# Kernel optimization log

Hardware: AMD Instinct MI355X
Metric: run time of the kernel (lower is better)

The kernel has to match this reference:

```python
import jax, jax.numpy as jnp
import numpy as np

H = 16  # num_heads
THETA = 10000.0


def apply_rope(x, positions, theta=THETA):
    # x: [..., S, d_k]; positions: [S]
    d_k = x.shape[-1]
    inv_freq = theta ** (-jnp.arange(0, d_k, 2, dtype=jnp.float32) / d_k)  # [d_k/2]
    ang = positions.astype(jnp.float32)[:, None] * inv_freq[None, :]  # [S, d_k/2]
    cos, sin = jnp.cos(ang), jnp.sin(ang)
    x1 = x[..., 0::2]
    x2 = x[..., 1::2]
    out_even = x1 * cos - x2 * sin
    out_odd = x1 * sin + x2 * cos
    out = jnp.stack([out_even, out_odd], axis=-1)  # [..., S, d_k/2, 2]
    return out.reshape(x.shape)


def setup_inputs() -> dict:
    key = jax.random.key(0)
    k1, k2, k3 = jax.random.split(key, 3)
    B, S, D = 2, 2048, 1024
    x = jax.random.normal(k1, (B, S, D), dtype=jnp.float32)
    token_positions = jnp.arange(S, dtype=jnp.int32)
    w_qkv = jax.random.normal(k2, (3 * D, D), dtype=jnp.float32) * (D ** -0.5)
    w_out = jax.random.normal(k3, (D, D), dtype=jnp.float32) * (D ** -0.5)
    return {"x": x, "token_positions": token_positions, "w_qkv": w_qkv, "w_out": w_out}


def reference(x, token_positions, w_qkv, w_out):
    B, S, D = x.shape
    d_k = D // H
    qkv = jnp.einsum('bsd,ed->bse', x, w_qkv)  # [B,S,3D]
    # split '(n h d_k)' -> n=3, h=H, d_k
    qkv = qkv.reshape(B, S, 3, H, d_k).transpose(2, 0, 3, 1, 4)  # [3,B,H,S,d_k]
    q = apply_rope(qkv[0], token_positions)
    k = apply_rope(qkv[1], token_positions)
    v = qkv[2]
    scale = 1.0 / jnp.sqrt(jnp.asarray(d_k, dtype=x.dtype))
    scores = jnp.einsum('bhqd,bhkd->bhqk', q, k) * scale  # [B,H,S,S]
    causal = jnp.tril(jnp.ones((S, S), dtype=bool))
    scores = jnp.where(causal, scores, jnp.asarray(-1e30, dtype=scores.dtype))
    attn = jax.nn.softmax(scores, axis=-1)
    out = jnp.einsum('bhqk,bhkd->bhqd', attn, v)  # [B,H,S,d_k]
    out = out.transpose(0, 2, 1, 3).reshape(B, S, D)  # merge (h d_v)
    return jnp.einsum('bsd,ed->bse', out, w_out)
```

## Files before the change

### kernel.cpp

```cpp
#include <hip/hip_runtime.h>

using bf16 = __bf16;
typedef __bf16 bf16x2 __attribute__((ext_vector_type(2)));
typedef __bf16 bf16x4v __attribute__((ext_vector_type(4)));
typedef __bf16 bf16x8 __attribute__((ext_vector_type(8)));
typedef float f32x4 __attribute__((ext_vector_type(4)));
typedef float floatx4 __attribute__((ext_vector_type(4)));

#define MFMA16(a, b, c) __builtin_amdgcn_mfma_f32_16x16x32_bf16((a), (b), (c), 0, 0, 0)

__device__ __forceinline__ float exp2a(float x) {
  float r;
  asm("v_exp_f32 %0, %1" : "=v"(r) : "v"(x));
  return r;
}

__global__ __launch_bounds__(256) void cast3_kernel(const float* __restrict__ a,
                                                    const float* __restrict__ b,
                                                    const float* __restrict__ c,
                                                    bf16* __restrict__ oa,
                                                    bf16* __restrict__ ob,
                                                    bf16* __restrict__ oc,
                                                    const int* __restrict__ pos,
                                                    float2* __restrict__ tab) {
  int i = blockIdx.x * 256 + threadIdx.x;
  if (i < 65536) {
    int s = i >> 5, ip = i & 31;
    float freq = exp2f(-(float)ip * (13.287712379549449f / 32.0f));
    float ang = (float)pos[s] * freq;
    float sn, cs;
    sincosf(ang, &sn, &cs);
    tab[i] = make_float2(cs, sn);
  }
  const float* in;
  bf16* out;
  int off;
  if (i < 1048576) {
    in = a; out = oa; off = i;
  } else if (i < 1835008) {
    in = b; out = ob; off = i - 1048576;
  } else {
    in = c; out = oc; off = i - 1835008;
  }
  floatx4 v = *(const floatx4*)(in + (size_t)off * 4);
  bf16x4v o;
  #pragma unroll
  for (int j = 0; j < 4; ++j) o[j] = (bf16)v[j];
  *(bf16x4v*)(out + (size_t)off * 4) = o;
}

template <bool OUT_F32, bool ROPE>
__global__ __launch_bounds__(256, 2) void gemm_bt(const bf16* __restrict__ A,
                                                  const bf16* __restrict__ B,
                                                  void* __restrict__ Cv,
                                                  int M, int N, int K,
                                                  const float2* __restrict__ tab) {
  __shared__ bf16 As[128 * 32];
  __shared__ bf16 Bs[128 * 32];
  const int t = threadIdx.x;
  const int l = t & 63;
  const int w = t >> 6;
  const int m0 = blockIdx.y * 128;
  const int n0 = blockIdx.x * 128;
  const int wr = (w >> 1) * 64;
  const int wc = (w & 1) * 64;
  const int lr = l & 15;
  const int lk = (l >> 4) * 8;

  f32x4 acc[4][4] = {};

  const int srow = t >> 2;
  const int scol = (t & 3) * 8;

  for (int k0 = 0; k0 < K; k0 += 32) {
    __syncthreads();
    #pragma unroll
    for (int j = 0; j < 2; ++j) {
      const bf16* ga = A + (size_t)(m0 + j * 64 + srow) * K + k0 + scol;
      __builtin_amdgcn_global_load_lds(
          (const __attribute__((address_space(1))) void*)ga,
          (__attribute__((address_space(3))) void*)(As + (j * 64 + srow) * 32 + scol),
          16, 0, 0);
      const bf16* gb = B + (size_t)(n0 + j * 64 + srow) * K + k0 + scol;
      __builtin_amdgcn_global_load_lds(
          (const __attribute__((address_space(1))) void*)gb,
          (__attribute__((address_space(3))) void*)(Bs + (j * 64 + srow) * 32 + scol),
          16, 0, 0);
    }
    __syncthreads();
    bf16x8 af[4], bfr[4];
    #pragma unroll
    for (int i = 0; i < 4; ++i) af[i] = *(const bf16x8*)(As + (wr + i * 16 + lr) * 32 + lk);
    #pragma unroll
    for (int i = 0; i < 4; ++i) bfr[i] = *(const bf16x8*)(Bs + (wc + i * 16 + lr) * 32 + lk);
    #pragma unroll
    for (int i = 0; i < 4; ++i)
      #pragma unroll
      for (int j = 0; j < 4; ++j)
        acc[i][j] = MFMA16(af[i], bfr[j], acc[i][j]);
  }

  const int cr0 = (l >> 4) * 4;
  const int cc = l & 15;

  if constexpr (ROPE) {
    if (n0 < 2048) {
      int ip[4];
      #pragma unroll
      for (int j = 0; j < 4; ++j) ip[j] = ((n0 + wc + j * 16 + cc) & 63) >> 1;
      const float sgn = (cc & 1) ? 1.f : -1.f;
      #pragma unroll
      for (int i = 0; i < 4; ++i) {
        #pragma unroll
        for (int r = 0; r < 4; ++r) {
          int row = m0 + wr + i * 16 + cr0 + r;
          int s = row & 2047;
          #pragma unroll
          for (int j = 0; j < 4; ++j) {
            float2 cs = tab[s * 32 + ip[j]];
            float self = acc[i][j][r];
            float partner = __shfl_xor(self, 1, 64);
            acc[i][j][r] = self * cs.x + sgn * cs.y * partner;
          }
        }
      }
    }
  }

  #pragma unroll
  for (int i = 0; i < 4; ++i) {
    #pragma unroll
    for (int j = 0; j < 4; ++j) {
      int row = m0 + wr + i * 16 + cr0;
      int col = n0 + wc + j * 16 + cc;
      #pragma unroll
      for (int r = 0; r < 4; ++r) {
        if constexpr (OUT_F32)
          ((float*)Cv)[(size_t)(row + r) * N + col] = acc[i][j][r];
        else
          ((bf16*)Cv)[(size_t)(row + r) * N + col] = (bf16)acc[i][j][r];
      }
    }
  }
}

__global__ __launch_bounds__(256, 4) void fa_causal(const bf16* __restrict__ qkv,
                                                    bf16* __restrict__ attn) {
  const int bh = blockIdx.x;
  const int b = bh >> 4, h = bh & 15;
  const int t = threadIdx.x, w = t >> 6, l = t & 63;
  const int lq = l & 15;
  const int g = l >> 4;
  const int lk = g * 8;
  const int swz = lq & 7;
  const int hz = lq >> 3;

  __shared__ bf16 Ks[2][64 * 64];
  __shared__ bf16 Vt[2][64 * 64];

  const size_t rs = 3072;
  const bf16* Qg = qkv + (size_t)(b * 2048) * rs + h * 64;
  const bf16* Kg = Qg + 1024;
  const bf16* Vg = Qg + 2048;

  const float SC = 0.125f * 1.44269504088896f;

  const int krow_in = l >> 3;
  const int kcsrc = (l & 7) ^ krow_in;
  const int kp = t >> 3;
  const int K0 = kp * 2;
  const int cd = t & 7;
  const int slot0 = (K0 & 32) | (((K0 >> 2) & 3) << 3) | (((K0 >> 4) & 1) << 2) | (K0 & 3);

  bf16x8 va, vb2;

  #define STAGE_K(KT, BUF)                                                                \
    {                                                                                     \
      _Pragma("unroll")                                                                   \
      for (int c = 0; c < 2; ++c) {                                                       \
        const int rowbase = w * 8 + c * 32;                                               \
        const bf16* src = Kg + (size_t)((KT)*64 + rowbase + krow_in) * rs + kcsrc * 8;    \
        __builtin_amdgcn_global_load_lds(                                                 \
            (const __attribute__((address_space(1))) void*)src,                           \
            (__attribute__((address_space(3))) void*)(&Ks[BUF][rowbase * 64]), 16, 0, 0); \
      }                                                                                   \
    }
  #define LOAD_V(KT)                                                          \
    {                                                                         \
      const bf16* vsrc = Vg + (size_t)((KT)*64 + K0) * rs + cd * 8;           \
      va = *(const bf16x8*)(vsrc);                                            \
      vb2 = *(const bf16x8*)(vsrc + rs);                                      \
    }
  #define WRITE_V(BUF)                                                        \
    {                                                                         \
      _Pragma("unroll")                                                       \
      for (int e = 0; e < 8; ++e) {                                           \
        bf16x2 pr;                                                            \
        pr[0] = va[e];                                                        \
        pr[1] = vb2[e];                                                       \
        *(bf16x2*)(&Vt[BUF][(cd * 8 + e) * 64 + (slot0 ^ ((e ^ cd) << 3))]) = pr; \
      }                                                                       \
    }

  #pragma unroll 1
  for (int seg = 0; seg < 2; ++seg) {
    const int qt = seg ? (31 - (int)blockIdx.y) : (int)blockIdx.y;
    const int q0 = qt * 64;
    const int qrow0 = q0 + w * 16;
    const int qg = qrow0 + lq;
    const int nkt = qt + 1;

    bf16x8 qfr[2];
    #pragma unroll
    for (int kk = 0; kk < 2; ++kk) {
      bf16x8 qv = *(const bf16x8*)(Qg + (size_t)qg * rs + kk * 32 + lk);
      #pragma unroll
      for (int j = 0; j < 8; ++j) qv[j] = (bf16)((float)qv[j] * SC);
      qfr[kk] = qv;
    }

    f32x4 o[4] = {};
    float mrow = -1e30f, lrow = 0.f;

    if (seg) __syncthreads();

    STAGE_K(0, 0)
    LOAD_V(0)
    WRITE_V(0)
    __syncthreads();

    for (int kt = 0; kt < nkt; ++kt) {
      const bool pf = (kt + 1 < nkt);
      if (pf) {
        LOAD_V(kt + 1)
        STAGE_K(kt + 1, (kt + 1) & 1)
      }

      if (kt * 64 <= qrow0 + 15) {
        const bf16* Kc = Ks[kt & 1];
        const bf16* Vc = Vt[kt & 1];
        const bool fullw = (kt * 64 + 63 <= qrow0);

        f32x4 sc[4] = {};
        __builtin_amdgcn_s_setprio(1);
        #pragma unroll
        for (int kf = 0; kf < 4; ++kf) {
          const int krow = kf * 16 + lq;
          bf16x8 kb0 = *(const bf16x8*)(&Kc[krow * 64 + ((0 + g) ^ swz) * 8]);
          bf16x8 kb1 = *(const bf16x8*)(&Kc[krow * 64 + ((4 + g) ^ swz) * 8]);
          sc[kf] = MFMA16(kb0, qfr[0], sc[kf]);
          sc[kf] = MFMA16(kb1, qfr[1], sc[kf]);
        }
        __builtin_amdgcn_s_setprio(0);

        float pv[16];
        if (fullw) {
          #pragma unroll
          for (int i = 0; i < 16; ++i) pv[i] = sc[i >> 2][i & 3];
        } else {
          #pragma unroll
          for (int kf = 0; kf < 4; ++kf)
            #pragma unroll
            for (int r = 0; r < 4; ++r) {
              int key = kt * 64 + kf * 16 + g * 4 + r;
              pv[kf * 4 + r] = (key <= qg) ? sc[kf][r] : -1e30f;
            }
        }
        float m0_ = fmaxf(pv[0], pv[1]), m1_ = fmaxf(pv[2], pv[3]);
        float m2_ = fmaxf(pv[4], pv[5]), m3_ = fmaxf(pv[6], pv[7]);
        float m4_ = fmaxf(pv[8], pv[9]), m5_ = fmaxf(pv[10], pv[11]);
        float m6_ = fmaxf(pv[12], pv[13]), m7_ = fmaxf(pv[14], pv[15]);
        float ma = fmaxf(fmaxf(m0_, m1_), fmaxf(m2_, m3_));
        float mb = fmaxf(fmaxf(m4_, m5_), fmaxf(m6_, m7_));
        float mxl = fmaxf(ma, mb);
        if (!__all(mxl <= mrow)) {
          float mx = fmaxf(mxl, __shfl_xor(mxl, 16, 64));
          mx = fmaxf(mx, __shfl_xor(mx, 32, 64));
          float mnew = fmaxf(mrow, mx);
          float al = exp2a(mrow - mnew);
          lrow *= al;
          #pragma unroll
          for (int fd = 0; fd < 4; ++fd)
            #pragma unroll
            for (int r = 0; r < 4; ++r) o[fd][r] *= al;
          mrow = mnew;
        }
        #pragma unroll
        for (int i = 0; i < 16; ++i) pv[i] = exp2a(pv[i] - mrow);
        float s0_ = pv[0] + pv[1], s1_ = pv[2] + pv[3];
        float s2_ = pv[4] + pv[5], s3_ = pv[6] + pv[7];
        float s4_ = pv[8] + pv[9], s5_ = pv[10] + pv[11];
        float s6_ = pv[12] + pv[13], s7_ = pv[14] + pv[15];
        float rsum = ((s0_ + s1_) + (s2_ + s3_)) + ((s4_ + s5_) + (s6_ + s7_));
        rsum += __shfl_xor(rsum, 16, 64);
        rsum += __shfl_xor(rsum, 32, 64);
        lrow += rsum;

        bf16x8 p0, p1;
        #pragma unroll
        for (int i = 0; i < 8; ++i) {
          p0[i] = (bf16)pv[i];
          p1[i] = (bf16)pv[8 + i];
        }

        __builtin_amdgcn_s_setprio(1);
        #pragma unroll
        for (int fd = 0; fd < 4; ++fd) {
          const int drow = fd * 16 + lq;
          {
            int pc = (0 * 4 + g) ^ swz ^ (fd << 1) ^ hz;
            bf16x8 vb = *(const bf16x8*)(&Vc[drow * 64 + pc * 8]);
            o[fd] = MFMA16(vb, p0, o[fd]);
          }
          {
            int pc = (1 * 4 + g) ^ swz ^ (fd << 1) ^ hz;
            bf16x8 vb = *(const bf16x8*)(&Vc[drow * 64 + pc * 8]);
            o[fd] = MFMA16(vb, p1, o[fd]);
          }
        }
        __builtin_amdgcn_s_setprio(0);
      }

      if (pf) {
        WRITE_V((kt + 1) & 1)
        __syncthreads();
      }
    }

    __syncthreads();
    bf16* Os = (bf16*)Ks + w * (16 * 72);
    float inv = 1.0f / lrow;
    #pragma unroll
    for (int fd = 0; fd < 4; ++fd) {
      bf16x4v ov;
      #pragma unroll
      for (int r = 0; r < 4; ++r) ov[r] = (bf16)(o[fd][r] * inv);
      *(bf16x4v*)(&Os[lq * 72 + fd * 16 + g * 4]) = ov;
    }
    asm volatile("" ::: "memory");
    #pragma unroll
    for (int p = 0; p < 2; ++p) {
      int idx = p * 64 + l;
      int row16 = idx >> 3, c8 = idx & 7;
      bf16x8 v = *(const bf16x8*)(&Os[row16 * 72 + c8 * 8]);
      *(bf16x8*)(&attn[(size_t)(b * 2048 + qrow0 + row16) * 1024 + h * 64 + c8 * 8]) = v;
    }
  }
}

extern "C" void kernel_launch(void* const* d_in, const int* in_sizes, int n_in,
                              void* d_out, int out_size, void* d_ws, size_t ws_size,
                              hipStream_t stream) {
  const float* x = (const float*)d_in[0];
  const int* pos = (const int*)d_in[1];
  const float* w_qkv = (const float*)d_in[2];
  const float* w_out = (const float*)d_in[3];
  float* out = (float*)d_out;

  char* ws = (char*)d_ws;
  bf16* xb   = (bf16*)(ws);
  bf16* wqb  = (bf16*)(ws + (8u << 20));
  bf16* wob  = (bf16*)(ws + (14u << 20));
  bf16* qkv  = (bf16*)(ws + (16u << 20));
  bf16* attn = (bf16*)(ws + (40u << 20));
  float2* tab = (float2*)(ws + (40u << 20));

  cast3_kernel<<<8192, 256, 0, stream>>>(x, w_qkv, w_out, xb, wqb, wob, pos, tab);

  dim3 g1(3072 / 128, 4096 / 128);
  gemm_bt<false, true><<<g1, 256, 0, stream>>>(xb, wqb, (void*)qkv, 4096, 3072, 1024, tab);

  dim3 gfa(32, 16);
  fa_causal<<<gfa, 256, 0, stream>>>(qkv, attn);

  dim3 g2(1024 / 128, 4096 / 128);
  gemm_bt<true, false><<<g2, 256, 0, stream>>>(attn, wob, (void*)out, 4096, 1024, 1024, nullptr);
}
```

Measured before the change: 118.8 us.

## Split causal attention KV range across two blocks and merge with combine kernel

```diff
diff --git a/kernel.cpp b/kernel.cpp
--- a/kernel.cpp
+++ b/kernel.cpp
@@ -144,10 +144,15 @@
   }
 }
 
-__global__ __launch_bounds__(256, 4) void fa_causal(const bf16* __restrict__ qkv,
-                                                    bf16* __restrict__ attn) {
+__global__ __launch_bounds__(256, 8) void fa_causal(const bf16* __restrict__ qkv,
+                                                    bf16* __restrict__ part0,
+                                                    bf16* __restrict__ part1,
+                                                    float2* __restrict__ ml) {
   const int bh = blockIdx.x;
   const int b = bh >> 4, h = bh & 15;
+  const int qt = 31 - (int)blockIdx.y;
+  const int q0 = qt * 64;
+  const int z = blockIdx.z;
   const int t = threadIdx.x, w = t >> 6, l = t & 63;
   const int lq = l & 15;
   const int g = l >> 4;
@@ -155,16 +160,30 @@
   const int swz = lq & 7;
   const int hz = lq >> 3;
 
-  __shared__ bf16 Ks[2][64 * 64];
-  __shared__ bf16 Vt[2][64 * 64];
+  __shared__ bf16 SH[2][64 * 64];
 
   const size_t rs = 3072;
   const bf16* Qg = qkv + (size_t)(b * 2048) * rs + h * 64;
   const bf16* Kg = Qg + 1024;
   const bf16* Vg = Qg + 2048;
 
+  const int qrow0 = q0 + w * 16;
+  const int qg = qrow0 + lq;
+
   const float SC = 0.125f * 1.44269504088896f;
-
+  bf16x8 qfr[2];
+  #pragma unroll
+  for (int kk = 0; kk < 2; ++kk) {
+    bf16x8 qv = *(const bf16x8*)(Qg + (size_t)qg * rs + kk * 32 + lk);
+    #pragma unroll
+    for (int j = 0; j < 8; ++j) qv[j] = (bf16)((float)qv[j] * SC);
+    qfr[kk] = qv;
+  }
+
+  f32x4 o[4] = {};
+  float mrow = -1e30f, lrow = 0.f;
+
+  const int nkt = qt + 1;
   const int krow_in = l >> 3;
   const int kcsrc = (l & 7) ^ krow_in;
   const int kp = t >> 3;
@@ -174,16 +193,16 @@
 
   bf16x8 va, vb2;
 
-  #define STAGE_K(KT, BUF)                                                                \
-    {                                                                                     \
-      _Pragma("unroll")                                                                   \
-      for (int c = 0; c < 2; ++c) {                                                       \
-        const int rowbase = w * 8 + c * 32;                                               \
-        const bf16* src = Kg + (size_t)((KT)*64 + rowbase + krow_in) * rs + kcsrc * 8;    \
-        __builtin_amdgcn_global_load_lds(                                                 \
-            (const __attribute__((address_space(1))) void*)src,                           \
-            (__attribute__((address_space(3))) void*)(&Ks[BUF][rowbase * 64]), 16, 0, 0); \
-      }                                                                                   \
+  #define STAGE_K(KT)                                                                   \
+    {                                                                                   \
+      _Pragma("unroll")                                                                 \
+      for (int c = 0; c < 2; ++c) {                                                     \
+        const int rowbase = w * 8 + c * 32;                                             \
+        const bf16* src = Kg + (size_t)((KT)*64 + rowbase + krow_in) * rs + kcsrc * 8;  \
+        __builtin_amdgcn_global_load_lds(                                               \
+            (const __attribute__((address_space(1))) void*)src,                         \
+            (__attribute__((address_space(3))) void*)(&SH[0][rowbase * 64]), 16, 0, 0); \
+      }                                                                                 \
     }
   #define LOAD_V(KT)                                                          \
     {                                                                         \
@@ -191,161 +210,154 @@
       va = *(const bf16x8*)(vsrc);                                            \
       vb2 = *(const bf16x8*)(vsrc + rs);                                      \
     }
-  #define WRITE_V(BUF)                                                        \
+  #define WRITE_V()                                                           \
     {                                                                         \
       _Pragma("unroll")                                                       \
       for (int e = 0; e < 8; ++e) {                                           \
         bf16x2 pr;                                                            \
         pr[0] = va[e];                                                        \
         pr[1] = vb2[e];                                                       \
-        *(bf16x2*)(&Vt[BUF][(cd * 8 + e) * 64 + (slot0 ^ ((e ^ cd) << 3))]) = pr; \
+        *(bf16x2*)(&SH[1][(cd * 8 + e) * 64 + (slot0 ^ ((e ^ cd) << 3))]) = pr; \
       }                                                                       \
     }
 
-  #pragma unroll 1
-  for (int seg = 0; seg < 2; ++seg) {
-    const int qt = seg ? (31 - (int)blockIdx.y) : (int)blockIdx.y;
-    const int q0 = qt * 64;
-    const int qrow0 = q0 + w * 16;
-    const int qg = qrow0 + lq;
-    const int nkt = qt + 1;
-
-    bf16x8 qfr[2];
-    #pragma unroll
-    for (int kk = 0; kk < 2; ++kk) {
-      bf16x8 qv = *(const bf16x8*)(Qg + (size_t)qg * rs + kk * 32 + lk);
-      #pragma unroll
-      for (int j = 0; j < 8; ++j) qv[j] = (bf16)((float)qv[j] * SC);
-      qfr[kk] = qv;
-    }
-
-    f32x4 o[4] = {};
-    float mrow = -1e30f, lrow = 0.f;
-
-    if (seg) __syncthreads();
-
-    STAGE_K(0, 0)
-    LOAD_V(0)
-    WRITE_V(0)
+  for (int kt = z; kt < nkt; kt += 2) {
+    if (kt != z) __syncthreads();
+    STAGE_K(kt)
+    LOAD_V(kt)
+    WRITE_V()
     __syncthreads();
 
-    for (int kt = 0; kt < nkt; ++kt) {
-      const bool pf = (kt + 1 < nkt);
-      if (pf) {
-        LOAD_V(kt + 1)
-        STAGE_K(kt + 1, (kt + 1) & 1)
-      }
-
-      if (kt * 64 <= qrow0 + 15) {
-        const bf16* Kc = Ks[kt & 1];
-        const bf16* Vc = Vt[kt & 1];
-        const bool fullw = (kt * 64 + 63 <= qrow0);
-
-        f32x4 sc[4] = {};
-        __builtin_amdgcn_s_setprio(1);
+    if (kt * 64 <= qrow0 + 15) {
+      const bf16* Kc = SH[0];
+      const bf16* Vc = SH[1];
+      const bool fullw = (kt * 64 + 63 <= qrow0);
+
+      f32x4 sc[4] = {};
+      __builtin_amdgcn_s_setprio(1);
+      #pragma unroll
+      for (int kf = 0; kf < 4; ++kf) {
+        const int krow = kf * 16 + lq;
+        bf16x8 kb0 = *(const bf16x8*)(&Kc[krow * 64 + ((0 + g) ^ swz) * 8]);
+        bf16x8 kb1 = *(const bf16x8*)(&Kc[krow * 64 + ((4 + g) ^ swz) * 8]);
+        sc[kf] = MFMA16(kb0, qfr[0], sc[kf]);
+        sc[kf] = MFMA16(kb1, qfr[1], sc[kf]);
+      }
+      __builtin_amdgcn_s_setprio(0);
+
+      float pv[16];
+      if (fullw) {
         #pragma unroll
-        for (int kf = 0; kf < 4; ++kf) {
-          const int krow = kf * 16 + lq;
-          bf16x8 kb0 = *(const bf16x8*)(&Kc[krow * 64 + ((0 + g) ^ swz) * 8]);
-          bf16x8 kb1 = *(const bf16x8*)(&Kc[krow * 64 + ((4 + g) ^ swz) * 8]);
-          sc[kf] = MFMA16(kb0, qfr[0], sc[kf]);
-          sc[kf] = MFMA16(kb1, qfr[1], sc[kf]);
+        for (int i = 0; i < 16; ++i) pv[i] = sc[i >> 2][i & 3];
+      } else {
+        #pragma unroll
+        for (int kf = 0; kf < 4; ++kf)
+          #pragma unroll
+          for (int r = 0; r < 4; ++r) {
+            int key = kt * 64 + kf * 16 + g * 4 + r;
+            pv[kf * 4 + r] = (key <= qg) ? sc[kf][r] : -1e30f;
+          }
+      }
+      float m0_ = fmaxf(pv[0], pv[1]), m1_ = fmaxf(pv[2], pv[3]);
+      float m2_ = fmaxf(pv[4], pv[5]), m3_ = fmaxf(pv[6], pv[7]);
+      float m4_ = fmaxf(pv[8], pv[9]), m5_ = fmaxf(pv[10], pv[11]);
+      float m6_ = fmaxf(pv[12], pv[13]), m7_ = fmaxf(pv[14], pv[15]);
+      float ma = fmaxf(fmaxf(m0_, m1_), fmaxf(m2_, m3_));
+      float mb = fmaxf(fmaxf(m4_, m5_), fmaxf(m6_, m7_));
+      float mxl = fmaxf(ma, mb);
+      if (!__all(mxl <= mrow)) {
+        float mx = fmaxf(mxl, __shfl_xor(mxl, 16, 64));
+        mx = fmaxf(mx, __shfl_xor(mx, 32, 64));
+        float mnew = fmaxf(mrow, mx);
+        float al = exp2a(mrow - mnew);
+        lrow *= al;
+        #pragma unroll
+        for (int fd = 0; fd < 4; ++fd)
+          #pragma unroll
+          for (int r = 0; r < 4; ++r) o[fd][r] *= al;
+        mrow = mnew;
+      }
+      #pragma unroll
+      for (int i = 0; i < 16; ++i) pv[i] = exp2a(pv[i] - mrow);
+      float s0_ = pv[0] + pv[1], s1_ = pv[2] + pv[3];
+      float s2_ = pv[4] + pv[5], s3_ = pv[6] + pv[7];
+      float s4_ = pv[8] + pv[9], s5_ = pv[10] + pv[11];
+      float s6_ = pv[12] + pv[13], s7_ = pv[14] + pv[15];
+      float rsum = ((s0_ + s1_) + (s2_ + s3_)) + ((s4_ + s5_) + (s6_ + s7_));
+      rsum += __shfl_xor(rsum, 16, 64);
+      rsum += __shfl_xor(rsum, 32, 64);
+      lrow += rsum;
+
+      bf16x8 p0, p1;
+      #pragma unroll
+      for (int i = 0; i < 8; ++i) {
+        p0[i] = (bf16)pv[i];
+        p1[i] = (bf16)pv[8 + i];
+      }
+
+      __builtin_amdgcn_s_setprio(1);
+      #pragma unroll
+      for (int fd = 0; fd < 4; ++fd) {
+        const int drow = fd * 16 + lq;
+        {
+          int pc = (0 * 4 + g) ^ swz ^ (fd << 1) ^ hz;
+          bf16x8 vb = *(const bf16x8*)(&Vc[drow * 64 + pc * 8]);
+          o[fd] = MFMA16(vb, p0, o[fd]);
         }
-        __builtin_amdgcn_s_setprio(0);
-
-        float pv[16];
-        if (fullw) {
-          #pragma unroll
-          for (int i = 0; i < 16; ++i) pv[i] = sc[i >> 2][i & 3];
-        } else {
-          #pragma unroll
-          for (int kf = 0; kf < 4; ++kf)
-            #pragma unroll
-            for (int r = 0; r < 4; ++r) {
-              int key = kt * 64 + kf * 16 + g * 4 + r;
-              pv[kf * 4 + r] = (key <= qg) ? sc[kf][r] : -1e30f;
-            }
+        {
+          int pc = (1 * 4 + g) ^ swz ^ (fd << 1) ^ hz;
+          bf16x8 vb = *(const bf16x8*)(&Vc[drow * 64 + pc * 8]);
+          o[fd] = MFMA16(vb, p1, o[fd]);
         }
-        float m0_ = fmaxf(pv[0], pv[1]), m1_ = fmaxf(pv[2], pv[3]);
-        float m2_ = fmaxf(pv[4], pv[5]), m3_ = fmaxf(pv[6], pv[7]);
-        float m4_ = fmaxf(pv[8], pv[9]), m5_ = fmaxf(pv[10], pv[11]);
-        float m6_ = fmaxf(pv[12], pv[13]), m7_ = fmaxf(pv[14], pv[15]);
-        float ma = fmaxf(fmaxf(m0_, m1_), fmaxf(m2_, m3_));
-        float mb = fmaxf(fmaxf(m4_, m5_), fmaxf(m6_, m7_));
-        float mxl = fmaxf(ma, mb);
-        if (!__all(mxl <= mrow)) {
-          float mx = fmaxf(mxl, __shfl_xor(mxl, 16, 64));
-          mx = fmaxf(mx, __shfl_xor(mx, 32, 64));
-          float mnew = fmaxf(mrow, mx);
-          float al = exp2a(mrow - mnew);
-          lrow *= al;
-          #pragma unroll
-          for (int fd = 0; fd < 4; ++fd)
-            #pragma unroll
-            for (int r = 0; r < 4; ++r) o[fd][r] *= al;
-          mrow = mnew;
-        }
-        #pragma unroll
-        for (int i = 0; i < 16; ++i) pv[i] = exp2a(pv[i] - mrow);
-        float s0_ = pv[0] + pv[1], s1_ = pv[2] + pv[3];
-        float s2_ = pv[4] + pv[5], s3_ = pv[6] + pv[7];
-        float s4_ = pv[8] + pv[9], s5_ = pv[10] + pv[11];
-        float s6_ = pv[12] + pv[13], s7_ = pv[14] + pv[15];
-        float rsum = ((s0_ + s1_) + (s2_ + s3_)) + ((s4_ + s5_) + (s6_ + s7_));
-        rsum += __shfl_xor(rsum, 16, 64);
-        rsum += __shfl_xor(rsum, 32, 64);
-        lrow += rsum;
-
-        bf16x8 p0, p1;
-        #pragma unroll
-        for (int i = 0; i < 8; ++i) {
-          p0[i] = (bf16)pv[i];
-          p1[i] = (bf16)pv[8 + i];
-        }
-
-        __builtin_amdgcn_s_setprio(1);
-        #pragma unroll
-        for (int fd = 0; fd < 4; ++fd) {
-          const int drow = fd * 16 + lq;
-          {
-            int pc = (0 * 4 + g) ^ swz ^ (fd << 1) ^ hz;
-            bf16x8 vb = *(const bf16x8*)(&Vc[drow * 64 + pc * 8]);
-            o[fd] = MFMA16(vb, p0, o[fd]);
-          }
-          {
-            int pc = (1 * 4 + g) ^ swz ^ (fd << 1) ^ hz;
-            bf16x8 vb = *(const bf16x8*)(&Vc[drow * 64 + pc * 8]);
-            o[fd] = MFMA16(vb, p1, o[fd]);
-          }
-        }
-        __builtin_amdgcn_s_setprio(0);
-      }
-
-      if (pf) {
-        WRITE_V((kt + 1) & 1)
-        __syncthreads();
-      }
-    }
-
-    __syncthreads();
-    bf16* Os = (bf16*)Ks + w * (16 * 72);
-    float inv = 1.0f / lrow;
-    #pragma unroll
-    for (int fd = 0; fd < 4; ++fd) {
-      bf16x4v ov;
-      #pragma unroll
-      for (int r = 0; r < 4; ++r) ov[r] = (bf16)(o[fd][r] * inv);
-      *(bf16x4v*)(&Os[lq * 72 + fd * 16 + g * 4]) = ov;
-    }
-    asm volatile("" ::: "memory");
-    #pragma unroll
-    for (int p = 0; p < 2; ++p) {
-      int idx = p * 64 + l;
-      int row16 = idx >> 3, c8 = idx & 7;
-      bf16x8 v = *(const bf16x8*)(&Os[row16 * 72 + c8 * 8]);
-      *(bf16x8*)(&attn[(size_t)(b * 2048 + qrow0 + row16) * 1024 + h * 64 + c8 * 8]) = v;
-    }
-  }
+      }
+      __builtin_amdgcn_s_setprio(0);
+    }
+  }
+
+  __syncthreads();
+  bf16* Obase = (z == 0) ? part0 : part1;
+  bf16* Os = (bf16*)SH + w * (16 * 72);
+  float inv = (lrow > 0.f) ? 1.0f / lrow : 0.f;
+  #pragma unroll
+  for (int fd = 0; fd < 4; ++fd) {
+    bf16x4v ov;
+    #pragma unroll
+    for (int r = 0; r < 4; ++r) ov[r] = (bf16)(o[fd][r] * inv);
+    *(bf16x4v*)(&Os[lq * 72 + fd * 16 + g * 4]) = ov;
+  }
+  if (g == 0)
+    ml[((size_t)z * 32 + bh) * 2048 + qrow0 + lq] = make_float2(mrow, lrow);
+  asm volatile("" ::: "memory");
+  #pragma unroll
+  for (int p = 0; p < 2; ++p) {
+    int idx = p * 64 + l;
+    int row16 = idx >> 3, c8 = idx & 7;
+    bf16x8 v = *(const bf16x8*)(&Os[row16 * 72 + c8 * 8]);
+    *(bf16x8*)(&Obase[(size_t)(b * 2048 + qrow0 + row16) * 1024 + h * 64 + c8 * 8]) = v;
+  }
+}
+
+__global__ __launch_bounds__(256) void combine_kernel(const bf16* __restrict__ p0,
+                                                      bf16* __restrict__ p1out,
+                                                      const float2* __restrict__ ml) {
+  int i = blockIdx.x * 256 + threadIdx.x;
+  size_t e4 = (size_t)i * 4;
+  int row = (int)(e4 >> 10), col = (int)(e4 & 1023);
+  int bhq = ((row >> 11) * 16 + (col >> 6)) * 2048 + (row & 2047);
+  float2 a0 = ml[bhq];
+  float2 a1 = ml[65536 + bhq];
+  float m = fmaxf(a0.x, a1.x);
+  float w0 = exp2a(a0.x - m) * a0.y;
+  float w1 = exp2a(a1.x - m) * a1.y;
+  float inv = 1.0f / (w0 + w1);
+  w0 *= inv;
+  w1 *= inv;
+  bf16x4v v0 = *(const bf16x4v*)(p0 + e4);
+  bf16x4v v1 = *(const bf16x4v*)(p1out + e4);
+  bf16x4v ov;
+  #pragma unroll
+  for (int j = 0; j < 4; ++j) ov[j] = (bf16)((float)v0[j] * w0 + (float)v1[j] * w1);
+  *(bf16x4v*)(p1out + e4) = ov;
 }
 
 extern "C" void kernel_launch(void* const* d_in, const int* in_sizes, int n_in,
@@ -364,14 +376,18 @@
   bf16* qkv  = (bf16*)(ws + (16u << 20));
   bf16* attn = (bf16*)(ws + (40u << 20));
   float2* tab = (float2*)(ws + (40u << 20));
+  bf16* part0 = xb;
+  float2* mlb = (float2*)wqb;
 
   cast3_kernel<<<8192, 256, 0, stream>>>(x, w_qkv, w_out, xb, wqb, wob, pos, tab);
 
   dim3 g1(3072 / 128, 4096 / 128);
   gemm_bt<false, true><<<g1, 256, 0, stream>>>(xb, wqb, (void*)qkv, 4096, 3072, 1024, tab);
 
-  dim3 gfa(32, 16);
-  fa_causal<<<gfa, 256, 0, stream>>>(qkv, attn);
+  dim3 gfa(32, 32, 2);
+  fa_causal<<<gfa, 256, 0, stream>>>(qkv, part0, attn, mlb);
+
+  combine_kernel<<<4096, 256, 0, stream>>>(part0, attn, mlb);
 
   dim3 g2(1024 / 128, 4096 / 128);
   gemm_bt<true, false><<<g2, 256, 0, stream>>>(attn, wob, (void*)out, 4096, 1024, 1024, nullptr);
```

New measurement: 157.2 us. +32.3%, slower.
